# Performance work log

Measured on AMD Instinct MI355X. Metric: run time of the kernel, lower is better.

The kernel has to match this reference:

```python
import jax, jax.numpy as jnp
import numpy as np


def _pairwise_sqdist(a, b):
    # a: [B,N,2], b: [B,M,2] -> [B,N,M] squared Euclidean distances
    a2 = jnp.sum(a * a, axis=-1)  # [B,N]
    b2 = jnp.sum(b * b, axis=-1)  # [B,M]
    ab = jnp.einsum('bnd,bmd->bnm', a, b)  # [B,N,M]
    return a2[:, :, None] + b2[:, None, :] - 2.0 * ab


def setup_inputs() -> dict:
    key = jax.random.key(0)
    k1, k2 = jax.random.split(key)
    B, N, M, D = 16, 2048, 2048, 2
    preds = jax.random.normal(k1, (B, N, D), dtype=jnp.float32)
    targs = jax.random.normal(k2, (B, M, D), dtype=jnp.float32)
    subcoef = jnp.ones((D,), dtype=jnp.float32)
    return {"preds": preds, "targs": targs, "subcoef": subcoef}


def reference(preds, targs, subcoef):
    # Bidirectional Chamfer-style NN L1 loss, faithful to NNLoss.nn_loss.
    d2 = _pairwise_sqdist(preds, targs)  # [B,N,M]

    # preds -> nearest GT (KDTree over targs queried with preds)
    nn_t = jnp.argmin(d2, axis=2)  # [B,N]
    matched_t = jnp.take_along_axis(targs, nn_t[:, :, None], axis=1)  # [B,N,2]
    move_preds_to_gt = jnp.sum(jnp.abs(preds - matched_t) * subcoef)

    # targs -> nearest pred (KDTree over preds queried with targs)
    nn_p = jnp.argmin(d2, axis=1)  # [B,M]
    matched_p = jnp.take_along_axis(preds, nn_p[:, :, None], axis=1)  # [B,M,2]
    move_gts_to_pred = jnp.sum(jnp.abs(matched_p - targs))

    return move_gts_to_pred + move_preds_to_gt
```

## Files before the change

### kernel.cpp

```cpp
#include <hip/hip_runtime.h>


typedef float v2f __attribute__((ext_vector_type(2)));
typedef float v4f __attribute__((ext_vector_type(4)));

constexpr int B      = 16;
constexpr int NPTS   = 2048;
constexpr int BLK    = 1024;
constexpr int G      = 256;
constexpr int S      = 16;
constexpr int QPT    = 4;
constexpr int SEGLEN = NPTS / S;
constexpr int QUADS  = SEGLEN / 4;
constexpr int NBLK   = 2 * B * (NPTS / G);

__global__ __launch_bounds__(BLK) void nn_main(
    const float* __restrict__ preds, const float* __restrict__ targs,
    const float* __restrict__ subcoef, float* __restrict__ out)
{
    __shared__ v4f xs4[NPTS / 4];
    __shared__ v4f ys4[NPTS / 4];
    __shared__ unsigned long long cand[S * G];
    __shared__ float ssum[BLK / 64];

    const int blk  = blockIdx.x;
    const int dir  = blk >> 7;
    const int b    = (blk >> 3) & 15;
    const int tile = blk & 7;

    const float2* qb = reinterpret_cast<const float2*>(dir == 0 ? preds : targs)
                       + b * NPTS + tile * G;
    const float2* db = reinterpret_cast<const float2*>(dir == 0 ? targs : preds)
                       + b * NPTS;

    const float4* db4 = reinterpret_cast<const float4*>(db);
    {
        const int j = threadIdx.x & 511;
        const float4 a = db4[2 * j];
        const float4 c = db4[2 * j + 1];
        if (threadIdx.x < 512) xs4[j] = {a.x, a.z, c.x, c.z};
        else                   ys4[j] = {a.y, a.w, c.y, c.w};
    }

    const int qslot = threadIdx.x & 63;
    const int seg   = threadIdx.x >> 6;

    v2f   m2x[QPT], m2y[QPT];
    float best[QPT];
    int   bj[QPT];
    #pragma unroll
    for (int q = 0; q < QPT; ++q) {
        const float2 qp = qb[qslot + q * 64];
        const float ax = -2.0f * qp.x, ay = -2.0f * qp.y;
        m2x[q] = {ax, ax};
        m2y[q] = {ay, ay};
        best[q] = 3.402823466e+38f;
        bj[q] = 0;
    }
    __syncthreads();

    const v4f* xsp = xs4 + seg * QUADS;
    const v4f* ysp = ys4 + seg * QUADS;
    #pragma unroll 8
    for (int i = 0; i < QUADS; ++i) {
        const v4f X = xsp[i];
        const v4f Y = ysp[i];
        const v2f xa = {X.x, X.y}, xb = {X.z, X.w};
        const v2f ya = {Y.x, Y.y}, yb = {Y.z, Y.w};
        const v2f t2a = __builtin_elementwise_fma(xa, xa, ya * ya);
        const v2f t2b = __builtin_elementwise_fma(xb, xb, yb * yb);
        #pragma unroll
        for (int q = 0; q < QPT; ++q) {
            const v2f da = __builtin_elementwise_fma(
                m2x[q], xa, __builtin_elementwise_fma(m2y[q], ya, t2a));
            const v2f dc = __builtin_elementwise_fma(
                m2x[q], xb, __builtin_elementwise_fma(m2y[q], yb, t2b));
            const v2f m2 = __builtin_elementwise_min(da, dc);
            const float dm = fminf(m2.x, m2.y);
            if (dm < best[q]) { best[q] = dm; bj[q] = i; }
        }
    }

    #pragma unroll
    for (int q = 0; q < QPT; ++q) {
        const v4f X = xsp[bj[q]];
        const v4f Y = ysp[bj[q]];
        const v2f xa = {X.x, X.y}, xb = {X.z, X.w};
        const v2f ya = {Y.x, Y.y}, yb = {Y.z, Y.w};
        const v2f t2a = __builtin_elementwise_fma(xa, xa, ya * ya);
        const v2f t2b = __builtin_elementwise_fma(xb, xb, yb * yb);
        const v2f da = __builtin_elementwise_fma(
            m2x[q], xa, __builtin_elementwise_fma(m2y[q], ya, t2a));
        const v2f dc = __builtin_elementwise_fma(
            m2x[q], xb, __builtin_elementwise_fma(m2y[q], yb, t2b));
        int off = 3;
        if (dc.x == best[q]) off = 2;
        if (da.y == best[q]) off = 1;
        if (da.x == best[q]) off = 0;
        const int idx = seg * SEGLEN + 4 * bj[q] + off;
        unsigned int fb = __float_as_uint(best[q]);
        fb ^= 0x80000000u | (unsigned int)((int)fb >> 31);
        cand[seg * G + qslot + q * 64] =
            ((unsigned long long)fb << 32) | (unsigned int)idx;
    }
    __syncthreads();

    float val = 0.0f;
    if (threadIdx.x < G) {
        unsigned long long bp = cand[threadIdx.x];
        #pragma unroll
        for (int s = 1; s < S; ++s) {
            const unsigned long long v = cand[s * G + threadIdx.x];
            bp = v < bp ? v : bp;
        }
        const int idx = (int)(unsigned int)bp;
        const float2 qp = qb[threadIdx.x];
        const float2 tp = db[idx];
        float sx = 1.0f, sy = 1.0f;
        if (dir == 0) { sx = subcoef[0]; sy = subcoef[1]; }
        val = fabsf(qp.x - tp.x) * sx + fabsf(qp.y - tp.y) * sy;
    }

    #pragma unroll
    for (int off = 32; off > 0; off >>= 1)
        val += __shfl_down(val, off, 64);
    if ((threadIdx.x & 63) == 0) ssum[threadIdx.x >> 6] = val;
    __syncthreads();
    if (threadIdx.x == 0) {
        float s = ssum[0];
        #pragma unroll
        for (int w = 1; w < BLK / 64; ++w) s += ssum[w];
        atomicAdd(out, s);
    }
}

extern "C" void kernel_launch(void* const* d_in, const int* in_sizes, int n_in,
                              void* d_out, int out_size, void* d_ws, size_t ws_size,
                              hipStream_t stream) {
    const float* preds   = (const float*)d_in[0];
    const float* targs   = (const float*)d_in[1];
    const float* subcoef = (const float*)d_in[2];
    float* out = (float*)d_out;

    nn_main<<<NBLK, BLK, 0, stream>>>(preds, targs, subcoef, out);
}
```

Baseline: 72.53 us.

## Track argmin per 16-point group and stage LDS per wave without block barrier

```diff
diff --git a/kernel.cpp b/kernel.cpp
--- a/kernel.cpp
+++ b/kernel.cpp
@@ -11,7 +11,8 @@
 constexpr int S      = 16;
 constexpr int QPT    = 4;
 constexpr int SEGLEN = NPTS / S;
-constexpr int QUADS  = SEGLEN / 4;
+constexpr int SQUADS = SEGLEN / 4;
+constexpr int HEXES  = SEGLEN / 16;
 constexpr int NBLK   = 2 * B * (NPTS / G);
 
 __global__ __launch_bounds__(BLK) void nn_main(
@@ -33,74 +34,86 @@
     const float2* db = reinterpret_cast<const float2*>(dir == 0 ? targs : preds)
                        + b * NPTS;
 
+    const int lane = threadIdx.x & 63;
+    const int seg  = threadIdx.x >> 6;
+
     const float4* db4 = reinterpret_cast<const float4*>(db);
     {
-        const int j = threadIdx.x & 511;
-        const float4 a = db4[2 * j];
-        const float4 c = db4[2 * j + 1];
-        if (threadIdx.x < 512) xs4[j] = {a.x, a.z, c.x, c.z};
-        else                   ys4[j] = {a.y, a.w, c.y, c.w};
+        const int j  = lane & 31;
+        const int gq = seg * SQUADS + j;
+        const float4 a = db4[2 * gq];
+        const float4 c = db4[2 * gq + 1];
+        if (lane < 32) xs4[gq] = {a.x, a.z, c.x, c.z};
+        else           ys4[gq] = {a.y, a.w, c.y, c.w};
     }
-
-    const int qslot = threadIdx.x & 63;
-    const int seg   = threadIdx.x >> 6;
 
     v2f   m2x[QPT], m2y[QPT];
     float best[QPT];
-    int   bj[QPT];
+    int   bh[QPT];
     #pragma unroll
     for (int q = 0; q < QPT; ++q) {
-        const float2 qp = qb[qslot + q * 64];
+        const float2 qp = qb[lane + q * 64];
         const float ax = -2.0f * qp.x, ay = -2.0f * qp.y;
         m2x[q] = {ax, ax};
         m2y[q] = {ay, ay};
         best[q] = 3.402823466e+38f;
-        bj[q] = 0;
+        bh[q] = 0;
     }
-    __syncthreads();
 
-    const v4f* xsp = xs4 + seg * QUADS;
-    const v4f* ysp = ys4 + seg * QUADS;
-    #pragma unroll 8
-    for (int i = 0; i < QUADS; ++i) {
-        const v4f X = xsp[i];
-        const v4f Y = ysp[i];
-        const v2f xa = {X.x, X.y}, xb = {X.z, X.w};
-        const v2f ya = {Y.x, Y.y}, yb = {Y.z, Y.w};
-        const v2f t2a = __builtin_elementwise_fma(xa, xa, ya * ya);
-        const v2f t2b = __builtin_elementwise_fma(xb, xb, yb * yb);
+    const v4f* xsp = xs4 + seg * SQUADS;
+    const v4f* ysp = ys4 + seg * SQUADS;
+    #pragma unroll
+    for (int h = 0; h < HEXES; ++h) {
+        v2f dmin[QPT];
+        #pragma unroll
+        for (int k = 0; k < 4; ++k) {
+            const v4f X = xsp[4 * h + k];
+            const v4f Y = ysp[4 * h + k];
+            const v2f xa = {X.x, X.y}, xb = {X.z, X.w};
+            const v2f ya = {Y.x, Y.y}, yb = {Y.z, Y.w};
+            const v2f t2a = __builtin_elementwise_fma(xa, xa, ya * ya);
+            const v2f t2b = __builtin_elementwise_fma(xb, xb, yb * yb);
+            #pragma unroll
+            for (int q = 0; q < QPT; ++q) {
+                const v2f da = __builtin_elementwise_fma(
+                    m2x[q], xa, __builtin_elementwise_fma(m2y[q], ya, t2a));
+                const v2f dc = __builtin_elementwise_fma(
+                    m2x[q], xb, __builtin_elementwise_fma(m2y[q], yb, t2b));
+                const v2f dq = __builtin_elementwise_min(da, dc);
+                dmin[q] = (k == 0) ? dq : __builtin_elementwise_min(dmin[q], dq);
+            }
+        }
         #pragma unroll
         for (int q = 0; q < QPT; ++q) {
-            const v2f da = __builtin_elementwise_fma(
-                m2x[q], xa, __builtin_elementwise_fma(m2y[q], ya, t2a));
-            const v2f dc = __builtin_elementwise_fma(
-                m2x[q], xb, __builtin_elementwise_fma(m2y[q], yb, t2b));
-            const v2f m2 = __builtin_elementwise_min(da, dc);
-            const float dm = fminf(m2.x, m2.y);
-            if (dm < best[q]) { best[q] = dm; bj[q] = i; }
+            const float dm = fminf(dmin[q].x, dmin[q].y);
+            if (dm < best[q]) { best[q] = dm; bh[q] = h; }
         }
     }
 
     #pragma unroll
     for (int q = 0; q < QPT; ++q) {
-        const v4f X = xsp[bj[q]];
-        const v4f Y = ysp[bj[q]];
-        const v2f xa = {X.x, X.y}, xb = {X.z, X.w};
-        const v2f ya = {Y.x, Y.y}, yb = {Y.z, Y.w};
-        const v2f t2a = __builtin_elementwise_fma(xa, xa, ya * ya);
-        const v2f t2b = __builtin_elementwise_fma(xb, xb, yb * yb);
-        const v2f da = __builtin_elementwise_fma(
-            m2x[q], xa, __builtin_elementwise_fma(m2y[q], ya, t2a));
-        const v2f dc = __builtin_elementwise_fma(
-            m2x[q], xb, __builtin_elementwise_fma(m2y[q], yb, t2b));
-        int off = 3;
-        if (dc.x == best[q]) off = 2;
-        if (da.y == best[q]) off = 1;
-        if (da.x == best[q]) off = 0;
-        const int idx = seg * SEGLEN + 4 * bj[q] + off;
+        int off = 0;
+        #pragma unroll
+        for (int k = 3; k >= 0; --k) {
+            const v4f X = xsp[4 * bh[q] + k];
+            const v4f Y = ysp[4 * bh[q] + k];
+            const v2f xa = {X.x, X.y}, xb = {X.z, X.w};
+            const v2f ya = {Y.x, Y.y}, yb = {Y.z, Y.w};
+            const v2f t2a = __builtin_elementwise_fma(xa, xa, ya * ya);
+            const v2f t2b = __builtin_elementwise_fma(xb, xb, yb * yb);
+            const v2f da = __builtin_elementwise_fma(
+                m2x[q], xa, __builtin_elementwise_fma(m2y[q], ya, t2a));
+            const v2f dc = __builtin_elementwise_fma(
+                m2x[q], xb, __builtin_elementwise_fma(m2y[q], yb, t2b));
+            if (dc.y == best[q]) off = 4 * k + 3;
+            if (dc.x == best[q]) off = 4 * k + 2;
+            if (da.y == best[q]) off = 4 * k + 1;
+            if (da.x == best[q]) off = 4 * k + 0;
+        }
+        const int idx = seg * SEGLEN + 16 * bh[q] + off;
         unsigned int fb = __float_as_uint(best[q]);
         fb ^= 0x80000000u | (unsigned int)((int)fb >> 31);
-        cand[seg * G + qslot + q * 64] =
+        cand[seg * G + lane + q * 64] =
             ((unsigned long long)fb << 32) | (unsigned int)idx;
     }
     __syncthreads();
```

Result: slower. 74.32 us (+2.5%).
